# Performance work log

Hardware: AMD Instinct MI355X
Metric: run time of the kernel (lower is better)

Reference implementation:

```python
import jax, jax.numpy as jnp
import numpy as np

N_NODES = 100000


def _sage_conv(x, src, dst, W_l, W_r, b, num_nodes):
    # PyG SAGEConv with mean aggregation:
    # out_i = (mean_{j: (j->i) in E} x_j) @ W_l + x_i @ W_r + b
    msg_sum = jax.ops.segment_sum(x[src], dst, num_segments=num_nodes)  # [N, F]
    deg = jax.ops.segment_sum(jnp.ones_like(src, dtype=x.dtype), dst, num_segments=num_nodes)
    agg = msg_sum / jnp.maximum(deg, 1.0)[:, None]
    return agg @ W_l + x @ W_r + b


def setup_inputs() -> dict:
    key = jax.random.key(0)
    k = jax.random.split(key, 7)
    F_IN, H, C = 128, 128, 14
    E = 1600000
    x = jax.random.normal(k[0], (N_NODES, F_IN), dtype=jnp.float32)
    edge_index = jax.random.randint(k[1], (2, E), 0, N_NODES, dtype=jnp.int64)
    s = 1.0 / np.sqrt(F_IN)
    W1_l = jax.random.normal(k[2], (F_IN, H), dtype=jnp.float32) * s
    W1_r = jax.random.normal(k[3], (F_IN, H), dtype=jnp.float32) * s
    b1 = jnp.zeros((H,), dtype=jnp.float32)
    sh = 1.0 / np.sqrt(H)
    W2_l = jax.random.normal(k[4], (H, C), dtype=jnp.float32) * sh
    W2_r = jax.random.normal(k[5], (H, C), dtype=jnp.float32) * sh
    b2 = jnp.zeros((C,), dtype=jnp.float32)
    return {"x": x, "edge_index": edge_index, "edge_SF_num": 6,
            "W1_l": W1_l, "W1_r": W1_r, "b1": b1,
            "W2_l": W2_l, "W2_r": W2_r, "b2": b2}


def reference(x, edge_index, edge_SF_num, W1_l, W1_r, b1, W2_l, W2_r, b2):
    src, dst = edge_index[0], edge_index[1]
    h = _sage_conv(x, src, dst, W1_l, W1_r, b1, N_NODES)
    h = jax.nn.relu(h)
    # dropout is identity at inference (training=False)
    out = _sage_conv(h, src, dst, W2_l, W2_r, b2, N_NODES)
    x_SF = jax.nn.log_softmax(out[:, :edge_SF_num], axis=1)
    x_Ptx = jax.nn.log_softmax(out[:, edge_SF_num:], axis=1)
    return (x_SF, x_Ptx)
```

## Files before the change

### kernel.cpp

```cpp
#include <hip/hip_runtime.h>
#include <hip/hip_bf16.h>

#define NN 100000
#define F 128
#define C_OUT 14
#define ZP 16
#define WIN 64
#define NWIN ((NN + WIN - 1) / WIN)
#define WCAP 1408
#define EBATCH 4096
#define HS 136
#define WPREPB 144

typedef __attribute__((ext_vector_type(8))) short v8s;
typedef __attribute__((ext_vector_type(4))) float v4f;
typedef __attribute__((ext_vector_type(2))) float v2f;

static __device__ __forceinline__ unsigned short f2bf(float f) {
    unsigned int u = __float_as_uint(f);
    unsigned int r = (u + 0x7fffu + ((u >> 16) & 1u)) >> 16;
    return (unsigned short)r;
}
static __device__ __forceinline__ unsigned int pack2(float a, float b) {
    return (unsigned int)f2bf(a) | ((unsigned int)f2bf(b) << 16);
}
static __device__ __forceinline__ void unpack2(unsigned int u, float& lo, float& hi) {
    lo = __uint_as_float(u << 16);
    hi = __uint_as_float(u & 0xffff0000u);
}
static __device__ __forceinline__ void accf8(const uint2 u, float* a) {
    v2f f0 = __builtin_amdgcn_cvt_pk_f32_fp8((int)u.x, false);
    a[0] += f0[0]; a[1] += f0[1];
    v2f f1 = __builtin_amdgcn_cvt_pk_f32_fp8((int)u.x, true);
    a[2] += f1[0]; a[3] += f1[1];
    v2f f2 = __builtin_amdgcn_cvt_pk_f32_fp8((int)u.y, false);
    a[4] += f2[0]; a[5] += f2[1];
    v2f f3 = __builtin_amdgcn_cvt_pk_f32_fp8((int)u.y, true);
    a[6] += f3[0]; a[7] += f3[1];
}
static __device__ __forceinline__ unsigned int bf4_to_fp8x4(const unsigned short* sp) {
    float f0, f1, f2, f3;
    unpack2(*(const unsigned int*)(sp + 0), f0, f1);
    unpack2(*(const unsigned int*)(sp + 2), f2, f3);
    unsigned int w = __builtin_amdgcn_cvt_pk_fp8_f32(f0, f1, 0, false);
    return __builtin_amdgcn_cvt_pk_fp8_f32(f2, f3, w, true);
}

__global__ __launch_bounds__(256) void prep_kernel(
    const int* __restrict__ src, const int* __restrict__ dst,
    unsigned* __restrict__ bucket, int* __restrict__ wcur, int E, int binBlocks,
    const float* __restrict__ W1l, const float* __restrict__ W1r,
    const float* __restrict__ W2l, const float* __restrict__ W2r,
    unsigned short* __restrict__ Wb, unsigned short* __restrict__ W2t)
{
    const int t = threadIdx.x;
    if ((int)blockIdx.x >= binBlocks) {
        const int idx = ((int)blockIdx.x - binBlocks) * 256 + t;
        if (idx < 2 * 128 * 128) {
            const int c   = idx >> 14;
            const int rem = idx & 16383;
            const int n   = rem >> 7;
            const int k   = rem & 127;
            const float* W = c ? W1r : W1l;
            Wb[idx] = f2bf(W[k * 128 + n]);
        } else if (idx < 2 * 128 * 128 + 32 * 128) {
            const int j = idx - 2 * 128 * 128;
            const int n = j >> 7;
            const int k = j & 127;
            float wv = 0.0f;
            if (n < 16) { if (n < C_OUT) wv = W2l[k * C_OUT + n]; }
            else        { if (n - 16 < C_OUT) wv = W2r[k * C_OUT + (n - 16)]; }
            W2t[j] = f2bf(wv);
        }
        return;
    }

    __shared__ int cnt_s[NWIN];
    __shared__ int gbase_s[NWIN];
    for (int w = t; w < NWIN; w += 256) cnt_s[w] = 0;
    __syncthreads();

    int      wreg[16];
    unsigned ereg[16];
    const int e0 = blockIdx.x * EBATCH;
    #pragma unroll
    for (int j = 0; j < 16; ++j) {
        const int e = e0 + j * 256 + t;
        int w = -1; unsigned ent = 0;
        if (e < E) {
            const int d = dst[e];
            const int s = src[e];
            w   = d >> 6;
            ent = ((unsigned)(d & (WIN - 1)) << 17) | (unsigned)s;
            atomicAdd(&cnt_s[w], 1);
        }
        wreg[j] = w; ereg[j] = ent;
    }
    __syncthreads();
    for (int w = t; w < NWIN; w += 256) {
        const int c = cnt_s[w];
        gbase_s[w] = c ? atomicAdd(&wcur[w], c) : 0;
    }
    __syncthreads();
    for (int w = t; w < NWIN; w += 256) cnt_s[w] = 0;
    __syncthreads();
    #pragma unroll
    for (int j = 0; j < 16; ++j) {
        const int w = wreg[j];
        if (w >= 0) {
            const int pos = gbase_s[w] + atomicAdd(&cnt_s[w], 1);
            if (pos < WCAP) bucket[(size_t)w * WCAP + pos] = ereg[j];
        }
    }
}

#define KSA 136
__global__ __launch_bounds__(256, 3) void pre1_kernel(
    const float* __restrict__ x, const unsigned short* __restrict__ Wb,
    const float* __restrict__ b1, unsigned char* __restrict__ pqa,
    unsigned short* __restrict__ pqs)
{
    __shared__ unsigned short A_s[64 * KSA];

    const int t    = threadIdx.x;
    const int m0   = blockIdx.x * 64;
    const int lane = t & 63;
    const int wave = t >> 6;
    const int lr   = lane & 15;
    const int quad = lane >> 4;
    const int nw0  = wave * 64;

    v8s bf[4][4];
    #pragma unroll
    for (int nt = 0; nt < 4; ++nt)
        #pragma unroll
        for (int ks = 0; ks < 4; ++ks)
            bf[nt][ks] = *(const v8s*)(Wb + (size_t)(nw0 + nt * 16 + lr) * 128 + ks * 32 + quad * 8);

    {
        const int mi = t & 63;
        const int ko = (t >> 6) * 32;
        const int m  = m0 + mi;
        unsigned short* dp = &A_s[mi * KSA + ko];
        if (m < NN) {
            const float4* sp = (const float4*)(x + (size_t)m * F + ko);
            #pragma unroll
            for (int j = 0; j < 8; j += 2) {
                const float4 f0 = sp[j], f1 = sp[j + 1];
                uint4 o;
                o.x = pack2(f0.x, f0.y); o.y = pack2(f0.z, f0.w);
                o.z = pack2(f1.x, f1.y); o.w = pack2(f1.z, f1.w);
                *(uint4*)(dp + j * 4) = o;
            }
        } else {
            #pragma unroll
            for (int j = 0; j < 4; ++j)
                *(uint4*)(dp + j * 8) = make_uint4(0u, 0u, 0u, 0u);
        }
    }
    __syncthreads();

    v4f acc[4][4];
    #pragma unroll
    for (int mt = 0; mt < 4; ++mt)
        #pragma unroll
        for (int nt = 0; nt < 4; ++nt)
            acc[mt][nt] = (v4f){0.f, 0.f, 0.f, 0.f};

    #pragma unroll
    for (int ks = 0; ks < 4; ++ks) {
        const int k0 = ks * 32 + quad * 8;
        #pragma unroll
        for (int mt = 0; mt < 4; ++mt) {
            const v8s a = *(const v8s*)&A_s[(mt * 16 + lr) * KSA + k0];
            acc[mt][0] = __builtin_amdgcn_mfma_f32_16x16x32_bf16(a, bf[0][ks], acc[mt][0], 0, 0, 0);
            acc[mt][1] = __builtin_amdgcn_mfma_f32_16x16x32_bf16(a, bf[1][ks], acc[mt][1], 0, 0, 0);
            acc[mt][2] = __builtin_amdgcn_mfma_f32_16x16x32_bf16(a, bf[2][ks], acc[mt][2], 0, 0, 0);
            acc[mt][3] = __builtin_amdgcn_mfma_f32_16x16x32_bf16(a, bf[3][ks], acc[mt][3], 0, 0, 0);
        }
    }
    __syncthreads();

    float bias[4];
    #pragma unroll
    for (int nt = 0; nt < 4; ++nt) {
        const int n = nw0 + nt * 16 + lr;
        bias[nt] = (n >= 128) ? b1[n - 128] : 0.0f;
    }

    unsigned short* C_s = A_s;
    #pragma unroll
    for (int p = 0; p < 2; ++p) {
        if ((nw0 >> 7) == p) {
            #pragma unroll
            for (int mt = 0; mt < 4; ++mt)
                #pragma unroll
                for (int nt = 0; nt < 4; ++nt) {
                    const int n = (nw0 & 127) + nt * 16 + lr;
                    #pragma unroll
                    for (int r = 0; r < 4; ++r) {
                        const int m = mt * 16 + quad * 4 + r;
                        C_s[m * KSA + n] = f2bf(acc[mt][nt][r] + bias[nt]);
                    }
                }
        }
        __syncthreads();
        if (p == 0) {
            const int mi8 = t >> 2;
            const int c0  = (t & 3) * 32;
            const int m   = m0 + mi8;
            if (m < NN) {
                unsigned char* dp = pqa + (size_t)m * 128 + c0;
                #pragma unroll
                for (int j = 0; j < 2; ++j) {
                    const unsigned short* sp = &C_s[mi8 * KSA + c0 + j * 16];
                    uint4 w;
                    w.x = bf4_to_fp8x4(sp + 0);
                    w.y = bf4_to_fp8x4(sp + 4);
                    w.z = bf4_to_fp8x4(sp + 8);
                    w.w = bf4_to_fp8x4(sp + 12);
                    *(uint4*)(dp + j * 16) = w;
                }
            }
        } else {
            const int mi = t >> 2;
            const int c0 = (t & 3) * 32;
            const int m  = m0 + mi;
            if (m < NN) {
                unsigned short* dp = pqs + (size_t)m * 128 + c0;
                const unsigned short* sp = &C_s[mi * KSA + c0];
                #pragma unroll
                for (int j = 0; j < 4; ++j)
                    *(uint4*)(dp + j * 8) = *(const uint4*)(sp + j * 8);
            }
        }
        __syncthreads();
    }
}

#define ISSUE8(U, B) { \
    const int s0_=(int)lp[(B)+0], s1_=(int)lp[(B)+1], s2_=(int)lp[(B)+2], s3_=(int)lp[(B)+3], \
              s4_=(int)lp[(B)+4], s5_=(int)lp[(B)+5], s6_=(int)lp[(B)+6], s7_=(int)lp[(B)+7]; \
    U##0=*(const uint2*)(pqa+(size_t)s0_*128+col); U##1=*(const uint2*)(pqa+(size_t)s1_*128+col); \
    U##2=*(const uint2*)(pqa+(size_t)s2_*128+col); U##3=*(const uint2*)(pqa+(size_t)s3_*128+col); \
    U##4=*(const uint2*)(pqa+(size_t)s4_*128+col); U##5=*(const uint2*)(pqa+(size_t)s5_*128+col); \
    U##6=*(const uint2*)(pqa+(size_t)s6_*128+col); U##7=*(const uint2*)(pqa+(size_t)s7_*128+col); }
#define PROC8(U) { accf8(U##0,a0); accf8(U##1,a1); accf8(U##2,a2); accf8(U##3,a3); \
                   accf8(U##4,a0); accf8(U##5,a1); accf8(U##6,a2); accf8(U##7,a3); }

__global__ __launch_bounds__(256, 4) void agg1f_kernel(
    const unsigned char* __restrict__ pqa, const unsigned short* __restrict__ pqs,
    unsigned* __restrict__ bucket, const int* __restrict__ wcur,
    const unsigned short* __restrict__ W2t, const float* __restrict__ b2,
    int* __restrict__ wbase, unsigned short* __restrict__ z, float* __restrict__ r)
{
    __shared__ unsigned list[WCAP];
    __shared__ int cnt_s[WIN], base_s[WIN], cur_s[WIN];
    __shared__ unsigned short hsm[WIN * HS];
    __shared__ unsigned short W2s[32 * HS];
    const int t  = threadIdx.x;
    const int wb = blockIdx.x;
    const int cntw = min(wcur[wb], WCAP);
    unsigned* bp = bucket + (size_t)wb * WCAP;

    {
        const int row = t >> 3;
        const int c16 = (t & 7) * 16;
        *(uint4*)&W2s[row * HS + c16]     = *(const uint4*)&W2t[row * 128 + c16];
        *(uint4*)&W2s[row * HS + c16 + 8] = *(const uint4*)&W2t[row * 128 + c16 + 8];
    }

    if (t < WIN) cnt_s[t] = 0;
    __syncthreads();
    for (int i = t; i < cntw; i += 256) atomicAdd(&cnt_s[bp[i] >> 17], 1);
    __syncthreads();
    if (t < WIN) base_s[t] = cnt_s[t];
    __syncthreads();
    for (int off = 1; off < WIN; off <<= 1) {
        int v = 0;
        if (t < WIN && t >= off) v = base_s[t - off];
        __syncthreads();
        if (t < WIN) base_s[t] += v;
        __syncthreads();
    }
    if (t < WIN) { const int b = base_s[t] - cnt_s[t]; base_s[t] = b; cur_s[t] = b; }
    __syncthreads();
    for (int i = t; i < cntw; i += 256) {
        const unsigned e = bp[i];
        list[atomicAdd(&cur_s[e >> 17], 1)] = e & 0x1FFFFu;
    }
    __syncthreads();

    for (int i = t; i < cntw; i += 256) bp[i] = list[i];
    if (t < WIN) wbase[wb * WIN + t] = base_s[t];

    const int g    = t >> 4;
    const int lane = t & 15;
    const int col  = lane * 8;
    #pragma unroll
    for (int rep = 0; rep < 4; ++rep) {
        const int nloc = rep * 16 + g;
        const int n = wb * WIN + nloc;
        if (n >= NN) continue;
        const int start = base_s[nloc];
        const int len   = cnt_s[nloc];
        float a0[8] = {0,0,0,0,0,0,0,0};
        float a1[8] = {0,0,0,0,0,0,0,0};
        float a2[8] = {0,0,0,0,0,0,0,0};
        float a3[8] = {0,0,0,0,0,0,0,0};
        const unsigned* lp = list + start;
        uint2 uA0,uA1,uA2,uA3,uA4,uA5,uA6,uA7;
        uint2 uB0,uB1,uB2,uB3,uB4,uB5,uB6,uB7;
        int i = 0;
        if (len >= 8) ISSUE8(uA, 0);
        for (; i + 24 <= len; i += 16) {
            ISSUE8(uB, i + 8);
            PROC8(uA);
            ISSUE8(uA, i + 16);
            PROC8(uB);
        }
        if (i + 16 <= len) {
            ISSUE8(uB, i + 8);
            PROC8(uA);
            PROC8(uB);
            i += 16;
        } else if (i + 8 <= len) {
            PROC8(uA);
            i += 8;
        }
        for (; i + 4 <= len; i += 4) {
            const int s0 = (int)lp[i + 0];
            const int s1 = (int)lp[i + 1];
            const int s2 = (int)lp[i + 2];
            const int s3 = (int)lp[i + 3];
            const uint2 u0 = *(const uint2*)(pqa + (size_t)s0 * 128 + col);
            const uint2 u1 = *(const uint2*)(pqa + (size_t)s1 * 128 + col);
            const uint2 u2 = *(const uint2*)(pqa + (size_t)s2 * 128 + col);
            const uint2 u3 = *(const uint2*)(pqa + (size_t)s3 * 128 + col);
            accf8(u0, a0); accf8(u1, a1); accf8(u2, a2); accf8(u3, a3);
        }
        for (; i < len; ++i) {
            const int s = (int)lp[i];
            const uint2 u = *(const uint2*)(pqa + (size_t)s * 128 + col);
            accf8(u, a0);
        }
        const float inv = 1.0f / (float)max(len, 1);
        const uint4 uq = *(const uint4*)(pqs + (size_t)n * 128 + lane * 8);
        float q[8];
        unpack2(uq.x, q[0], q[1]); unpack2(uq.y, q[2], q[3]);
        unpack2(uq.z, q[4], q[5]); unpack2(uq.w, q[6], q[7]);
        float hv[8];
        #pragma unroll
        for (int j = 0; j < 8; ++j)
            hv[j] = fmaxf((a0[j] + a1[j] + a2[j] + a3[j]) * inv + q[j], 0.0f);
        uint4 o;
        o.x = pack2(hv[0], hv[1]);
        o.y = pack2(hv[2], hv[3]);
        o.z = pack2(hv[4], hv[5]);
        o.w = pack2(hv[6], hv[7]);
        *(uint4*)&hsm[nloc * HS + lane * 8] = o;
    }
    __syncthreads();

    {
        const int wave = t >> 6;
        const int l64  = t & 63;
        const int lr   = l64 & 15;
        const int quad = l64 >> 4;
        const int m0w  = wave * 16;
        v4f accz = (v4f){0.f, 0.f, 0.f, 0.f};
        v4f accr = (v4f){0.f, 0.f, 0.f, 0.f};
        #pragma unroll
        for (int kt = 0; kt < 4; ++kt) {
            const int k0 = kt * 32 + quad * 8;
            const v8s a  = *(const v8s*)&hsm[(m0w + lr) * HS + k0];
            const v8s bz = *(const v8s*)&W2s[lr * HS + k0];
            const v8s br = *(const v8s*)&W2s[(16 + lr) * HS + k0];
            accz = __builtin_amdgcn_mfma_f32_16x16x32_bf16(a, bz, accz, 0, 0, 0);
            accr = __builtin_amdgcn_mfma_f32_16x16x32_bf16(a, br, accr, 0, 0, 0);
        }
        const float b2v = (lr < C_OUT) ? b2[lr] : 0.0f;
        #pragma unroll
        for (int rr = 0; rr < 4; ++rr) {
            const int m = m0w + quad * 4 + rr;
            const int n = wb * WIN + m;
            if (n < NN) {
                z[(size_t)n * ZP + lr] = f2bf(accz[rr]);
                r[(size_t)n * ZP + lr] = accr[rr] + b2v;
            }
        }
    }
}

__global__ __launch_bounds__(256) void agg2s_kernel(
    const unsigned short* __restrict__ z, const float* __restrict__ r,
    const unsigned* __restrict__ bucket, const int* __restrict__ wcur,
    const int* __restrict__ wbase, const int* __restrict__ sf_ptr,
    float* __restrict__ out)
{
    __shared__ unsigned list[WCAP];
    __shared__ int base_s[WIN + 1];
    __shared__ float sm[WIN][ZP + 1];
    const int t  = threadIdx.x;
    const int wb = blockIdx.x;
    const int cntw = min(wcur[wb], WCAP);
    const unsigned* bp = bucket + (size_t)wb * WCAP;

    if (t < WIN) base_s[t] = wbase[wb * WIN + t];
    if (t == 0) base_s[WIN] = cntw;
    for (int i = t; i < cntw; i += 256) list[i] = bp[i];
    __syncthreads();

    const int g  = t >> 2;
    const int j4 = (t & 3) * 4;
    const int n  = wb * WIN + g;
    if (n < NN) {
        const int start = base_s[g];
        const int len   = base_s[g + 1] - base_s[g];
        float4 a0 = make_float4(0.f, 0.f, 0.f, 0.f);
        float4 a1 = a0, a2 = a0, a3 = a0;
        int i = 0;
        for (; i + 8 <= len; i += 8) {
            const int s0 = (int)list[start + i + 0];
            const int s1 = (int)list[start + i + 1];
            const int s2 = (int)list[start + i + 2];
            const int s3 = (int)list[start + i + 3];
            const int s4 = (int)list[start + i + 4];
            const int s5 = (int)list[start + i + 5];
            const int s6 = (int)list[start + i + 6];
            const int s7 = (int)list[start + i + 7];
            const uint2 u0 = *(const uint2*)(z + (size_t)s0 * ZP + j4);
            const uint2 u1 = *(const uint2*)(z + (size_t)s1 * ZP + j4);
            const uint2 u2 = *(const uint2*)(z + (size_t)s2 * ZP + j4);
            const uint2 u3 = *(const uint2*)(z + (size_t)s3 * ZP + j4);
            const uint2 u4 = *(const uint2*)(z + (size_t)s4 * ZP + j4);
            const uint2 u5 = *(const uint2*)(z + (size_t)s5 * ZP + j4);
            const uint2 u6 = *(const uint2*)(z + (size_t)s6 * ZP + j4);
            const uint2 u7 = *(const uint2*)(z + (size_t)s7 * ZP + j4);
            float f0, f1, f2, f3;
            unpack2(u0.x, f0, f1); unpack2(u0.y, f2, f3);
            a0.x += f0; a0.y += f1; a0.z += f2; a0.w += f3;
            unpack2(u1.x, f0, f1); unpack2(u1.y, f2, f3);
            a1.x += f0; a1.y += f1; a1.z += f2; a1.w += f3;
            unpack2(u2.x, f0, f1); unpack2(u2.y, f2, f3);
            a2.x += f0; a2.y += f1; a2.z += f2; a2.w += f3;
            unpack2(u3.x, f0, f1); unpack2(u3.y, f2, f3);
            a3.x += f0; a3.y += f1; a3.z += f2; a3.w += f3;
            unpack2(u4.x, f0, f1); unpack2(u4.y, f2, f3);
            a0.x += f0; a0.y += f1; a0.z += f2; a0.w += f3;
            unpack2(u5.x, f0, f1); unpack2(u5.y, f2, f3);
            a1.x += f0; a1.y += f1; a1.z += f2; a1.w += f3;
            unpack2(u6.x, f0, f1); unpack2(u6.y, f2, f3);
            a2.x += f0; a2.y += f1; a2.z += f2; a2.w += f3;
            unpack2(u7.x, f0, f1); unpack2(u7.y, f2, f3);
            a3.x += f0; a3.y += f1; a3.z += f2; a3.w += f3;
        }
        for (; i + 4 <= len; i += 4) {
            const int s0 = (int)list[start + i + 0];
            const int s1 = (int)list[start + i + 1];
            const int s2 = (int)list[start + i + 2];
            const int s3 = (int)list[start + i + 3];
            const uint2 u0 = *(const uint2*)(z + (size_t)s0 * ZP + j4);
            const uint2 u1 = *(const uint2*)(z + (size_t)s1 * ZP + j4);
            const uint2 u2 = *(const uint2*)(z + (size_t)s2 * ZP + j4);
            const uint2 u3 = *(const uint2*)(z + (size_t)s3 * ZP + j4);
            float f0, f1, f2, f3;
            unpack2(u0.x, f0, f1); unpack2(u0.y, f2, f3);
            a0.x += f0; a0.y += f1; a0.z += f2; a0.w += f3;
            unpack2(u1.x, f0, f1); unpack2(u1.y, f2, f3);
            a1.x += f0; a1.y += f1; a1.z += f2; a1.w += f3;
            unpack2(u2.x, f0, f1); unpack2(u2.y, f2, f3);
            a2.x += f0; a2.y += f1; a2.z += f2; a2.w += f3;
            unpack2(u3.x, f0, f1); unpack2(u3.y, f2, f3);
            a3.x += f0; a3.y += f1; a3.z += f2; a3.w += f3;
        }
        for (; i < len; ++i) {
            const int s = (int)list[start + i];
            const uint2 u = *(const uint2*)(z + (size_t)s * ZP + j4);
            float f0, f1, f2, f3;
            unpack2(u.x, f0, f1); unpack2(u.y, f2, f3);
            a0.x += f0; a0.y += f1; a0.z += f2; a0.w += f3;
        }
        const float inv = 1.0f / (float)max(len, 1);
        const float4 rv = *(const float4*)(r + (size_t)n * ZP + j4);
        sm[g][j4 + 0] = (a0.x + a1.x + a2.x + a3.x) * inv + rv.x;
        sm[g][j4 + 1] = (a0.y + a1.y + a2.y + a3.y) * inv + rv.y;
        sm[g][j4 + 2] = (a0.z + a1.z + a2.z + a3.z) * inv + rv.z;
        sm[g][j4 + 3] = (a0.w + a1.w + a2.w + a3.w) * inv + rv.w;
    }
    __syncthreads();

    if (t < WIN) {
        const int n2 = wb * WIN + t;
        if (n2 < NN) {
            const int sf = *sf_ptr;
            const float* row = sm[t];
            float m = -1e30f;
            for (int c = 0; c < sf; ++c) m = fmaxf(m, row[c]);
            float s = 0.0f;
            for (int c = 0; c < sf; ++c) s += expf(row[c] - m);
            float ls = m + logf(s);
            for (int c = 0; c < sf; ++c)
                out[(long long)n2 * sf + c] = row[c] - ls;
            m = -1e30f;
            for (int c = sf; c < C_OUT; ++c) m = fmaxf(m, row[c]);
            s = 0.0f;
            for (int c = sf; c < C_OUT; ++c) s += expf(row[c] - m);
            ls = m + logf(s);
            const int pt = C_OUT - sf;
            for (int c = sf; c < C_OUT; ++c)
                out[(long long)NN * sf + (long long)n2 * pt + (c - sf)] = row[c] - ls;
        }
    }
}

extern "C" void kernel_launch(void* const* d_in, const int* in_sizes, int n_in,
                              void* d_out, int out_size, void* d_ws, size_t ws_size,
                              hipStream_t stream)
{
    const float* x   = (const float*)d_in[0];
    const int*   ei  = (const int*)d_in[1];
    const int*   sfp = (const int*)d_in[2];
    const float* W1l = (const float*)d_in[3];
    const float* W1r = (const float*)d_in[4];
    const float* b1  = (const float*)d_in[5];
    const float* W2l = (const float*)d_in[6];
    const float* W2r = (const float*)d_in[7];
    const float* b2  = (const float*)d_in[8];
    float*       out = (float*)d_out;

    const int E = in_sizes[1] / 2;
    const int* src = ei;
    const int* dst = ei + E;

    int*      wcur   = (int*)d_ws;
    int*      wbase  = wcur + 2048;
    unsigned* bucket = (unsigned*)(wbase + NWIN * WIN);
    unsigned short* Wb  = (unsigned short*)(bucket + (size_t)NWIN * WCAP);
    unsigned short* W2t = Wb + 2 * 128 * 128;
    unsigned short* pqs = W2t + 32 * 128;
    unsigned char*  pqa = (unsigned char*)(pqs + (size_t)NN * 128);
    unsigned short* z   = (unsigned short*)(pqa + (size_t)NN * 128);
    float*          r   = (float*)(z + (size_t)NN * ZP);

    hipMemsetAsync(wcur, 0, 2048 * sizeof(int), stream);

    const int binBlocks = (E + EBATCH - 1) / EBATCH;
    prep_kernel<<<binBlocks + WPREPB, 256, 0, stream>>>(
        src, dst, bucket, wcur, E, binBlocks, W1l, W1r, W2l, W2r, Wb, W2t);

    pre1_kernel<<<(NN + 63) / 64, 256, 0, stream>>>(x, Wb, b1, pqa, pqs);

    agg1f_kernel<<<NWIN, 256, 0, stream>>>(pqa, pqs, bucket, wcur, W2t, b2, wbase, z, r);

    agg2s_kernel<<<NWIN, 256, 0, stream>>>(z, r, bucket, wcur, wbase, sfp, out);
}
```

Measured before the change: 219.9 us.

## Replace window binning with per-node count, scan, and direct CSR scatter

Edge bucketing now runs as three steps. A global per-node degree count with atomics is followed by a per-window wavefront scan, then each edge is scattered straight to its node's CSR slot using per-node atomic cursors. The per-window local sort, scan and bucket rewrite inside agg1f are gone, and agg1f's occupancy hint rises from 4 to 5 blocks per CU. The cost is two extra launches, more global atomics spread over 100k counters, and reading the full WCAP list even when a window holds fewer edges.

```diff
diff --git a/kernel.cpp b/kernel.cpp
--- a/kernel.cpp
+++ b/kernel.cpp
@@ -46,9 +46,8 @@
     return __builtin_amdgcn_cvt_pk_fp8_f32(f2, f3, w, true);
 }
 
-__global__ __launch_bounds__(256) void prep_kernel(
-    const int* __restrict__ src, const int* __restrict__ dst,
-    unsigned* __restrict__ bucket, int* __restrict__ wcur, int E, int binBlocks,
+__global__ __launch_bounds__(256) void prepA_kernel(
+    const int* __restrict__ dst, int* __restrict__ dcnt, int E, int binBlocks,
     const float* __restrict__ W1l, const float* __restrict__ W1r,
     const float* __restrict__ W2l, const float* __restrict__ W2r,
     unsigned short* __restrict__ Wb, unsigned short* __restrict__ W2t)
@@ -74,42 +73,48 @@
         }
         return;
     }
-
-    __shared__ int cnt_s[NWIN];
-    __shared__ int gbase_s[NWIN];
-    for (int w = t; w < NWIN; w += 256) cnt_s[w] = 0;
-    __syncthreads();
-
-    int      wreg[16];
-    unsigned ereg[16];
     const int e0 = blockIdx.x * EBATCH;
     #pragma unroll
     for (int j = 0; j < 16; ++j) {
         const int e = e0 + j * 256 + t;
-        int w = -1; unsigned ent = 0;
+        if (e < E) atomicAdd(&dcnt[dst[e]], 1);
+    }
+}
+
+__global__ __launch_bounds__(256) void scan_kernel(
+    const int* __restrict__ dcnt, int* __restrict__ gbase, int* __restrict__ ncur)
+{
+    const int t    = threadIdx.x;
+    const int widx = blockIdx.x * 4 + (t >> 6);
+    if (widx >= NWIN) return;
+    const int lane = t & 63;
+    const int n    = widx * WIN + lane;
+    const int c    = dcnt[n];
+    int v = c;
+    #pragma unroll
+    for (int off = 1; off < WIN; off <<= 1) {
+        const int u = __shfl_up(v, off, WIN);
+        if (lane >= off) v += u;
+    }
+    const int ex = v - c;
+    const int b  = widx * WCAP + min(ex, WCAP);
+    gbase[n] = b;
+    ncur[n]  = b;
+}
+
+__global__ __launch_bounds__(256) void prepB_kernel(
+    const int* __restrict__ src, const int* __restrict__ dst,
+    int* __restrict__ ncur, unsigned* __restrict__ bucket, int E)
+{
+    const int e0 = blockIdx.x * EBATCH;
+    #pragma unroll
+    for (int j = 0; j < 16; ++j) {
+        const int e = e0 + j * 256 + threadIdx.x;
         if (e < E) {
             const int d = dst[e];
-            const int s = src[e];
-            w   = d >> 6;
-            ent = ((unsigned)(d & (WIN - 1)) << 17) | (unsigned)s;
-            atomicAdd(&cnt_s[w], 1);
-        }
-        wreg[j] = w; ereg[j] = ent;
-    }
-    __syncthreads();
-    for (int w = t; w < NWIN; w += 256) {
-        const int c = cnt_s[w];
-        gbase_s[w] = c ? atomicAdd(&wcur[w], c) : 0;
-    }
-    __syncthreads();
-    for (int w = t; w < NWIN; w += 256) cnt_s[w] = 0;
-    __syncthreads();
-    #pragma unroll
-    for (int j = 0; j < 16; ++j) {
-        const int w = wreg[j];
-        if (w >= 0) {
-            const int pos = gbase_s[w] + atomicAdd(&cnt_s[w], 1);
-            if (pos < WCAP) bucket[(size_t)w * WCAP + pos] = ereg[j];
+            const int pos = atomicAdd(&ncur[d], 1);
+            if (pos < (d >> 6) * WCAP + WCAP)
+                bucket[pos] = (unsigned)src[e];
         }
     }
 }
@@ -248,20 +253,19 @@
 #define PROC8(U) { accf8(U##0,a0); accf8(U##1,a1); accf8(U##2,a2); accf8(U##3,a3); \
                    accf8(U##4,a0); accf8(U##5,a1); accf8(U##6,a2); accf8(U##7,a3); }
 
-__global__ __launch_bounds__(256, 4) void agg1f_kernel(
+__global__ __launch_bounds__(256, 5) void agg1f_kernel(
     const unsigned char* __restrict__ pqa, const unsigned short* __restrict__ pqs,
-    unsigned* __restrict__ bucket, const int* __restrict__ wcur,
-    const unsigned short* __restrict__ W2t, const float* __restrict__ b2,
-    int* __restrict__ wbase, unsigned short* __restrict__ z, float* __restrict__ r)
+    const unsigned* __restrict__ bucket, const int* __restrict__ gbase,
+    const int* __restrict__ dcnt, const unsigned short* __restrict__ W2t,
+    const float* __restrict__ b2, unsigned short* __restrict__ z, float* __restrict__ r)
 {
     __shared__ unsigned list[WCAP];
-    __shared__ int cnt_s[WIN], base_s[WIN], cur_s[WIN];
+    __shared__ int base_s[WIN], cnt_s[WIN];
     __shared__ unsigned short hsm[WIN * HS];
     __shared__ unsigned short W2s[32 * HS];
     const int t  = threadIdx.x;
     const int wb = blockIdx.x;
-    const int cntw = min(wcur[wb], WCAP);
-    unsigned* bp = bucket + (size_t)wb * WCAP;
+    const unsigned* bp = bucket + (size_t)wb * WCAP;
 
     {
         const int row = t >> 3;
@@ -269,30 +273,14 @@
         *(uint4*)&W2s[row * HS + c16]     = *(const uint4*)&W2t[row * 128 + c16];
         *(uint4*)&W2s[row * HS + c16 + 8] = *(const uint4*)&W2t[row * 128 + c16 + 8];
     }
-
-    if (t < WIN) cnt_s[t] = 0;
+    if (t < WIN) {
+        const int n    = wb * WIN + t;
+        const int brel = gbase[n] - wb * WCAP;
+        base_s[t] = brel;
+        cnt_s[t]  = min(dcnt[n], WCAP - brel);
+    }
+    for (int i = t; i < WCAP; i += 256) list[i] = bp[i];
     __syncthreads();
-    for (int i = t; i < cntw; i += 256) atomicAdd(&cnt_s[bp[i] >> 17], 1);
-    __syncthreads();
-    if (t < WIN) base_s[t] = cnt_s[t];
-    __syncthreads();
-    for (int off = 1; off < WIN; off <<= 1) {
-        int v = 0;
-        if (t < WIN && t >= off) v = base_s[t - off];
-        __syncthreads();
-        if (t < WIN) base_s[t] += v;
-        __syncthreads();
-    }
-    if (t < WIN) { const int b = base_s[t] - cnt_s[t]; base_s[t] = b; cur_s[t] = b; }
-    __syncthreads();
-    for (int i = t; i < cntw; i += 256) {
-        const unsigned e = bp[i];
-        list[atomicAdd(&cur_s[e >> 17], 1)] = e & 0x1FFFFu;
-    }
-    __syncthreads();
-
-    for (int i = t; i < cntw; i += 256) bp[i] = list[i];
-    if (t < WIN) wbase[wb * WIN + t] = base_s[t];
 
     const int g    = t >> 4;
     const int lane = t & 15;
@@ -394,21 +382,24 @@
 
 __global__ __launch_bounds__(256) void agg2s_kernel(
     const unsigned short* __restrict__ z, const float* __restrict__ r,
-    const unsigned* __restrict__ bucket, const int* __restrict__ wcur,
-    const int* __restrict__ wbase, const int* __restrict__ sf_ptr,
+    const unsigned* __restrict__ bucket, const int* __restrict__ gbase,
+    const int* __restrict__ dcnt, const int* __restrict__ sf_ptr,
     float* __restrict__ out)
 {
     __shared__ unsigned list[WCAP];
-    __shared__ int base_s[WIN + 1];
+    __shared__ int base_s[WIN], cnt_s[WIN];
     __shared__ float sm[WIN][ZP + 1];
     const int t  = threadIdx.x;
     const int wb = blockIdx.x;
-    const int cntw = min(wcur[wb], WCAP);
     const unsigned* bp = bucket + (size_t)wb * WCAP;
 
-    if (t < WIN) base_s[t] = wbase[wb * WIN + t];
-    if (t == 0) base_s[WIN] = cntw;
-    for (int i = t; i < cntw; i += 256) list[i] = bp[i];
+    if (t < WIN) {
+        const int n    = wb * WIN + t;
+        const int brel = gbase[n] - wb * WCAP;
+        base_s[t] = brel;
+        cnt_s[t]  = min(dcnt[n], WCAP - brel);
+    }
+    for (int i = t; i < WCAP; i += 256) list[i] = bp[i];
     __syncthreads();
 
     const int g  = t >> 2;
@@ -416,7 +407,7 @@
     const int n  = wb * WIN + g;
     if (n < NN) {
         const int start = base_s[g];
-        const int len   = base_s[g + 1] - base_s[g];
+        const int len   = cnt_s[g];
         float4 a0 = make_float4(0.f, 0.f, 0.f, 0.f);
         float4 a1 = a0, a2 = a0, a3 = a0;
         int i = 0;
@@ -533,9 +524,10 @@
     const int* src = ei;
     const int* dst = ei + E;
 
-    int*      wcur   = (int*)d_ws;
-    int*      wbase  = wcur + 2048;
-    unsigned* bucket = (unsigned*)(wbase + NWIN * WIN);
+    int*      dcnt   = (int*)d_ws;
+    int*      gbase  = dcnt + NWIN * WIN;
+    int*      ncur   = gbase + NWIN * WIN;
+    unsigned* bucket = (unsigned*)(ncur + NWIN * WIN);
     unsigned short* Wb  = (unsigned short*)(bucket + (size_t)NWIN * WCAP);
     unsigned short* W2t = Wb + 2 * 128 * 128;
     unsigned short* pqs = W2t + 32 * 128;
@@ -543,15 +535,20 @@
     unsigned short* z   = (unsigned short*)(pqa + (size_t)NN * 128);
     float*          r   = (float*)(z + (size_t)NN * ZP);
 
-    hipMemsetAsync(wcur, 0, 2048 * sizeof(int), stream);
+    hipMemsetAsync(dcnt, 0, (size_t)NWIN * WIN * sizeof(int), stream);
 
     const int binBlocks = (E + EBATCH - 1) / EBATCH;
-    prep_kernel<<<binBlocks + WPREPB, 256, 0, stream>>>(
-        src, dst, bucket, wcur, E, binBlocks, W1l, W1r, W2l, W2r, Wb, W2t);
+
+    prepA_kernel<<<binBlocks + WPREPB, 256, 0, stream>>>(
+        dst, dcnt, E, binBlocks, W1l, W1r, W2l, W2r, Wb, W2t);
+
+    scan_kernel<<<(NWIN + 3) / 4, 256, 0, stream>>>(dcnt, gbase, ncur);
+
+    prepB_kernel<<<binBlocks, 256, 0, stream>>>(src, dst, ncur, bucket, E);
 
     pre1_kernel<<<(NN + 63) / 64, 256, 0, stream>>>(x, Wb, b1, pqa, pqs);
 
-    agg1f_kernel<<<NWIN, 256, 0, stream>>>(pqa, pqs, bucket, wcur, W2t, b2, wbase, z, r);
-
-    agg2s_kernel<<<NWIN, 256, 0, stream>>>(z, r, bucket, wcur, wbase, sfp, out);
-}
+    agg1f_kernel<<<NWIN, 256, 0, stream>>>(pqa, pqs, bucket, gbase, dcnt, W2t, b2, z, r);
+
+    agg2s_kernel<<<NWIN, 256, 0, stream>>>(z, r, bucket, gbase, dcnt, sfp, out);
+}
```

Result: slower. 415.4 us (+88.9%).
